# Kernel optimization log

Measured on AMD Instinct MI355X. Metric: run time of the kernel, lower is better.

Reference implementation:

```python
import jax, jax.numpy as jnp
import numpy as np

N_E = 16384      # codebook size
E_DIM = 32       # codebook vector dim (== channel dim of z)
BETA = 0.25      # commitment loss weight
ENT_RATIO = 0.1  # entropy loss ratio
TEMP = 0.01      # entropy loss temperature


def _l2norm(x, eps=1e-12):
    # matches F.normalize(p=2, dim=-1): x / max(||x||, eps)
    n = jnp.sqrt(jnp.sum(x * x, axis=-1, keepdims=True))
    return x / jnp.maximum(n, eps)


def _entropy_loss(affinity):
    # affinity: (T, N_E)
    fa = affinity / TEMP
    probs = jax.nn.softmax(fa, axis=-1)
    log_probs = jax.nn.log_softmax(fa + 1e-05, axis=-1)
    avg_probs = jnp.mean(probs, axis=0)
    avg_entropy = -jnp.sum(avg_probs * jnp.log(avg_probs + 1e-05))
    sample_entropy = -jnp.mean(jnp.sum(probs * log_probs, axis=-1))
    return sample_entropy - avg_entropy


def setup_inputs() -> dict:
    key = jax.random.key(0)
    k1, k2 = jax.random.split(key)
    z = jax.random.normal(k1, (32, E_DIM, 16, 16), dtype=jnp.float32)
    # torch init: uniform(-1/n_e, 1/n_e) then l2-normalized rows
    emb = jax.random.uniform(k2, (N_E, E_DIM), dtype=jnp.float32,
                             minval=-1.0 / N_E, maxval=1.0 / N_E)
    emb = _l2norm(emb)
    return {"z": z, "embedding": emb}


def reference(z, embedding):
    # z: (b, c, h, w) -> (b, h, w, c)
    zb = jnp.transpose(z, (0, 2, 3, 1))
    zb = _l2norm(zb)                       # l2_norm=True path
    zf = zb.reshape(-1, E_DIM)             # (T, d), T = b*h*w
    emb = _l2norm(embedding)               # (N_E, d)
    # squared L2 distances (cdist expansion)
    d = (jnp.sum(zf * zf, axis=1, keepdims=True)
         + jnp.sum(emb * emb, axis=1)
         - 2.0 * jnp.einsum('td,nd->tn', zf, emb))   # (T, N_E)
    idx = jnp.argmin(d, axis=1)            # (T,)
    z_q = emb[idx].reshape(zb.shape)       # (b, h, w, c)
    # training losses
    vq_loss = jnp.mean((z_q - jax.lax.stop_gradient(zb)) ** 2)
    commit_loss = BETA * jnp.mean((jax.lax.stop_gradient(z_q) - zb) ** 2)
    entropy_loss = ENT_RATIO * _entropy_loss(-d)
    # straight-through estimator
    z_q_st = zb + jax.lax.stop_gradient(z_q - zb)
    out = jnp.transpose(z_q_st, (0, 3, 1, 2))  # back to (b, c, h, w)
    return out, vq_loss, commit_loss, entropy_loss
```

## Files before the change

kernel.cpp:

```cpp
#include <hip/hip_runtime.h>


#define N_E 16384
#define ED 32
#define T 8192
#define NS1 16
#define SKIPM -36.0f
#define PHT 16

#define K2 288.53900817779268f
#define NS2F -144.26950408889634f
#define BIAS1 -208.53900817779268f
#define LN2 0.6931471805599453f

typedef __attribute__((ext_vector_type(8))) short s16x8;
typedef __attribute__((ext_vector_type(4))) float f32x4;

__device__ __forceinline__ float fexp2(float x) { return __builtin_amdgcn_exp2f(x); }
__device__ __forceinline__ float flog2(float x) { return __builtin_amdgcn_logf(x); }
__device__ __forceinline__ float fmed3(float a, float b, float c) {
  return __builtin_amdgcn_fmed3f(a, b, c);
}

__device__ __forceinline__ float midband(float key) {
  return __uint_as_float((__float_as_uint(key) & 0xFFFFFC00u) | 512u);
}

__device__ __forceinline__ void gload16(const void* g, void* l) {
  __builtin_amdgcn_global_load_lds(
      (const __attribute__((address_space(1))) void*)g,
      (__attribute__((address_space(3))) void*)l, 16, 0, 0);
}

__device__ __forceinline__ unsigned short f2bf(float x) {
  unsigned u = __float_as_uint(x);
  unsigned r = (u + 0x7FFFu + ((u >> 16) & 1u)) >> 16;
  return (unsigned short)r;
}
__device__ __forceinline__ float bf2f(unsigned short h) {
  return __uint_as_float(((unsigned)h) << 16);
}

__device__ __forceinline__ void split_store_t(short* __restrict__ base,
    int row, int g, float4 va, float4 vb, float sc) {
  float f[8] = { va.x * sc, va.y * sc, va.z * sc, va.w * sc,
                 vb.x * sc, vb.y * sc, vb.z * sc, vb.w * sc };
  s16x8 H, L;
#pragma unroll
  for (int e = 0; e < 8; ++e) {
    unsigned short h = f2bf(f[e]);
    H[e] = (short)h;
    L[e] = (short)f2bf(f[e] - bf2f(h));
  }
  s16x8* p = (s16x8*)base;
  const int tile = row >> 4, c = row & 15;
  p[tile * 128 + g * 16 + c] = H;
  p[tile * 128 + 64 + g * 16 + c] = L;
}

__device__ __forceinline__ void split_store_h(short* __restrict__ base,
    int row, int g, float4 va, float4 vb) {
  float f[8] = { va.x, va.y, va.z, va.w, vb.x, vb.y, vb.z, vb.w };
  s16x8 H;
#pragma unroll
  for (int e = 0; e < 8; ++e) H[e] = (short)f2bf(f[e]);
  ((s16x8*)base)[(row >> 4) * 64 + g * 16 + (row & 15)] = H;
}

__global__ __launch_bounds__(256) void k_prep(const float* __restrict__ emb,
    const float* __restrict__ z, float* __restrict__ embn,
    float* __restrict__ ses2, float* __restrict__ zf, float* __restrict__ a02,
    short* __restrict__ ehl, short* __restrict__ zhl, float* __restrict__ avg,
    float* __restrict__ scal) {
  if (blockIdx.x < 64) {
    int n = blockIdx.x * 256 + threadIdx.x;
    const float4* r4 = (const float4*)(emb + (size_t)n * ED);
    float4 v[8]; float s = 0.f;
#pragma unroll
    for (int j = 0; j < 8; ++j) {
      v[j] = r4[j];
      s = fmaf(v[j].x, v[j].x, s); s = fmaf(v[j].y, v[j].y, s);
      s = fmaf(v[j].z, v[j].z, s); s = fmaf(v[j].w, v[j].w, s);
    }
    float inv = 1.0f / fmaxf(sqrtf(s), 1e-12f);
    float s2 = 0.f;
    float4* o4 = (float4*)(embn + (size_t)n * ED);
#pragma unroll
    for (int j = 0; j < 8; ++j) {
      float4 w; w.x = v[j].x * inv; w.y = v[j].y * inv;
      w.z = v[j].z * inv; w.w = v[j].w * inv;
      o4[j] = w; v[j] = w;
      s2 = fmaf(w.x, w.x, s2); s2 = fmaf(w.y, w.y, s2);
      s2 = fmaf(w.z, w.z, s2); s2 = fmaf(w.w, w.w, s2);
    }
    ses2[n] = NS2F * s2;
#pragma unroll
    for (int g = 0; g < 4; ++g)
      split_store_h(ehl, n, g, v[2 * g], v[2 * g + 1]);
  } else if (blockIdx.x < 96) {
    int t = (blockIdx.x - 64) * 256 + threadIdx.x;
    int b = t >> 8, hw = t & 255;
    const float* base = z + (size_t)b * (ED * 256) + hw;
    float4 v[8]; float s = 0.f;
#pragma unroll
    for (int j = 0; j < 8; ++j) {
      float4 w;
      w.x = base[(4 * j + 0) * 256]; w.y = base[(4 * j + 1) * 256];
      w.z = base[(4 * j + 2) * 256]; w.w = base[(4 * j + 3) * 256];
      v[j] = w;
      s = fmaf(w.x, w.x, s); s = fmaf(w.y, w.y, s);
      s = fmaf(w.z, w.z, s); s = fmaf(w.w, w.w, s);
    }
    float inv = 1.0f / fmaxf(sqrtf(s), 1e-12f);
    float s2 = 0.f;
    float4* o4 = (float4*)(zf + (size_t)t * ED);
#pragma unroll
    for (int j = 0; j < 8; ++j) {
      float4 w; w.x = v[j].x * inv; w.y = v[j].y * inv;
      w.z = v[j].z * inv; w.w = v[j].w * inv;
      o4[j] = w; v[j] = w;
      s2 = fmaf(w.x, w.x, s2); s2 = fmaf(w.y, w.y, s2);
      s2 = fmaf(w.z, w.z, s2); s2 = fmaf(w.w, w.w, s2);
    }
    a02[t] = NS2F * s2;
#pragma unroll
    for (int g = 0; g < 4; ++g)
      split_store_t(zhl, t, g, v[2 * g], v[2 * g + 1], K2);
  } else if (blockIdx.x < 160) {
    avg[(blockIdx.x - 96) * 256 + threadIdx.x] = 0.f;
  } else {
    if (threadIdx.x < 4) scal[threadIdx.x] = 0.f;
  }
}

__global__ __launch_bounds__(256, 4) void k_pass1(
    const short* __restrict__ ehl, const short* __restrict__ zhl,
    float* __restrict__ cand1, float* __restrict__ cand2) {
  const int tid = threadIdx.x;
  const int lane = tid & 63, wv = tid >> 6;
  const int q = lane >> 4, c = lane & 15;
  const int rowbase = blockIdx.x * 128 + wv * 32;
  const int NT = (N_E / NS1) / 16;
  const int NP = NT / PHT;

  __shared__ s16x8 dbuf[2][PHT * 64];

  const s16x8* zg = (const s16x8*)zhl;
  const int atile = rowbase >> 4;
  s16x8 ah[2], al[2];
#pragma unroll
  for (int rg = 0; rg < 2; ++rg) {
    ah[rg] = zg[(atile + rg) * 128 + lane];
    al[rg] = zg[(atile + rg) * 128 + 64 + lane];
  }

  f32x4 bias;
#pragma unroll
  for (int r = 0; r < 4; ++r) bias[r] = BIAS1;

  float m1[2][4], m2[2][4];
#pragma unroll
  for (int rg = 0; rg < 2; ++rg)
#pragma unroll
    for (int k = 0; k < 4; ++k) { m1[rg][k] = -1e30f; m2[rg][k] = -1e30f; }

  const s16x8* eg = (const s16x8*)ehl + (size_t)blockIdx.y * (64 * 64);

#pragma unroll
  for (int j = 0; j < 4; ++j)
    gload16(eg + wv * 256 + j * 64 + lane, &dbuf[0][wv * 256 + j * 64]);
  __syncthreads();

  for (int p = 0; p < NP; ++p) {
    if (p + 1 < NP) {
      const s16x8* gs = eg + (p + 1) * (PHT * 64);
      s16x8* lb = &dbuf[(p + 1) & 1][0];
#pragma unroll
      for (int j = 0; j < 4; ++j)
        gload16(gs + wv * 256 + j * 64 + lane, lb + wv * 256 + j * 64);
    }
    const s16x8* bb = &dbuf[p & 1][0];
#pragma unroll
    for (int tt = 0; tt < PHT; ++tt) {
      s16x8 bh = bb[tt * 64 + lane];
      const unsigned tuc = (((unsigned)(p * PHT + tt)) << 4) | (unsigned)c;

      f32x4 acc0 = __builtin_amdgcn_mfma_f32_16x16x32_bf16(ah[0], bh, bias, 0, 0, 0);
      acc0 = __builtin_amdgcn_mfma_f32_16x16x32_bf16(al[0], bh, acc0, 0, 0, 0);
      f32x4 acc1 = __builtin_amdgcn_mfma_f32_16x16x32_bf16(ah[1], bh, bias, 0, 0, 0);
      acc1 = __builtin_amdgcn_mfma_f32_16x16x32_bf16(al[1], bh, acc1, 0, 0, 0);

#pragma unroll
      for (int r = 0; r < 4; ++r) {
        float k0 = __uint_as_float((__float_as_uint(acc0[r]) & 0xFFFFFC00u) | tuc);
        m2[0][r] = fmed3(k0, m1[0][r], m2[0][r]);
        m1[0][r] = fmaxf(m1[0][r], k0);
        float k1v = __uint_as_float((__float_as_uint(acc1[r]) & 0xFFFFFC00u) | tuc);
        m2[1][r] = fmed3(k1v, m1[1][r], m2[1][r]);
        m1[1][r] = fmaxf(m1[1][r], k1v);
      }
    }
    __syncthreads();
  }

  const int s = blockIdx.y;
#pragma unroll
  for (int rg = 0; rg < 2; ++rg) {
    float4 v1 = make_float4(m1[rg][0], m1[rg][1], m1[rg][2], m1[rg][3]);
    float4 v2 = make_float4(m2[rg][0], m2[rg][1], m2[rg][2], m2[rg][3]);
    const size_t base = (size_t)(s * 16 + c) * T + (rowbase + rg * 16 + q * 4);
    *(float4*)(cand1 + base) = v1;
    *(float4*)(cand2 + base) = v2;
  }
}

__global__ __launch_bounds__(256) void k_fin(
    const float* __restrict__ cand1, const float* __restrict__ cand2,
    const float* __restrict__ zf, const float* __restrict__ embn,
    const float* __restrict__ ses2, const float* __restrict__ a02,
    float* __restrict__ avg, float* __restrict__ scal,
    float* __restrict__ out) {
  const int tid = threadIdx.x;
  const int rr = tid & 15;
  const int g  = tid >> 4;
  const int row = blockIdx.x * 16 + rr;

  __shared__ float sZ[256], sS2[256], sk1[256];
  __shared__ unsigned long long rbest[16];
  __shared__ float slZ[16], sth[16], rsE[16], rvq[16];
  if (tid < 16) rbest[tid] = 0ull;

  float ka[16], kb[16];
  float k1 = -1e30f, Z = 0.f, S2 = 0.f;
#pragma unroll
  for (int k = 0; k < 16; ++k) {
    const int u = g * 16 + k;
    const float ca = cand1[(size_t)u * T + row];
    const float cb = cand2[(size_t)u * T + row];
    ka[k] = ca; kb[k] = cb;
    k1 = fmaxf(k1, ca);
    const float fa = midband(ca), fb = midband(cb);
    const float ea = fexp2(fa), eb = fexp2(fb);
    Z += ea + eb;
    S2 = fmaf(ea, fa, fmaf(eb, fb, S2));
  }
  sZ[tid] = Z; sS2[tid] = S2; sk1[tid] = k1;
  __syncthreads();
  for (int st = 8; st >= 1; st >>= 1) {
    if (g < st) {
      const int o = tid + st * 16;
      sZ[tid] += sZ[o]; sS2[tid] += sS2[o];
      sk1[tid] = fmaxf(sk1[tid], sk1[o]);
    }
    __syncthreads();
  }
  if (g == 0) { slZ[rr] = flog2(sZ[rr]); sth[rr] = sk1[rr] - 2.5f; }
  __syncthreads();
  const float lZ = slZ[rr], thr = sth[rr];
  const float a02t = a02[row];

#pragma unroll
  for (int k = 0; k < 16; ++k) {
    const int u = g * 16 + k;
#pragma unroll
    for (int h = 0; h < 2; ++h) {
      const float key = h ? kb[k] : ka[k];
      const unsigned kid = __float_as_uint(key) & 1023u;
      const int idx = (u >> 4) * 1024 + (int)((kid >> 4) << 4) + (int)(kid & 15u);
      const float dl = midband(key) - lZ;
      if (dl > SKIPM) atomicAdd(&avg[idx], fexp2(dl));
      if (key > thr) {
        const float4* er = (const float4*)(embn + (size_t)idx * ED);
        const float4* zr = (const float4*)(zf + (size_t)row * ED);
        float d = 0.f;
#pragma unroll
        for (int j = 0; j < 8; ++j) {
          float4 a = er[j], b = zr[j];
          d = fmaf(a.x, b.x, d); d = fmaf(a.y, b.y, d);
          d = fmaf(a.z, b.z, d); d = fmaf(a.w, b.w, d);
        }
        const float fbx = fmaf(K2, d, a02t + ses2[idx]);
        const unsigned ub = __float_as_uint(fbx);
        const unsigned ord = ub ^ (unsigned)(((int)ub >> 31) | 0x80000000);
        const unsigned long long pk =
            ((unsigned long long)ord << 14) | (unsigned long long)(16383 - idx);
        atomicMax(&rbest[rr], pk);
      }
    }
  }
  __syncthreads();

  if (g == 0) {
    rsE[rr] = sS2[rr] / sZ[rr] - lZ;
    const int bi = 16383 - (int)(rbest[rr] & 16383ull);

    const float4* zr4 = (const float4*)(zf + (size_t)row * ED);
    float4 z0 = zr4[0], z1 = zr4[1], z2 = zr4[2], z3 = zr4[3];
    float4 z4 = zr4[4], z5 = zr4[5], z6 = zr4[6], z7 = zr4[7];

    const int b = row >> 8, hw = row & 255;
    float* ob = out + (size_t)b * (ED * 256) + hw;
    float ss = 0.f;
    const float4* e4 = (const float4*)(embn + (size_t)bi * ED);
#pragma unroll
    for (int j = 0; j < 8; ++j) {
      float4 qv = e4[j];
      float4 zv = (j == 0) ? z0 : (j == 1) ? z1 : (j == 2) ? z2 : (j == 3) ? z3
                : (j == 4) ? z4 : (j == 5) ? z5 : (j == 6) ? z6 : z7;
      float df;
      df = qv.x - zv.x; ss = fmaf(df, df, ss); ob[(4 * j + 0) * 256] = zv.x + (qv.x - zv.x);
      df = qv.y - zv.y; ss = fmaf(df, df, ss); ob[(4 * j + 1) * 256] = zv.y + (qv.y - zv.y);
      df = qv.z - zv.z; ss = fmaf(df, df, ss); ob[(4 * j + 2) * 256] = zv.z + (qv.z - zv.z);
      df = qv.w - zv.w; ss = fmaf(df, df, ss); ob[(4 * j + 3) * 256] = zv.w + (qv.w - zv.w);
    }
    rvq[rr] = ss;
  }
  __syncthreads();
  if (tid == 0) {
    float se = 0.f, vq = 0.f;
    for (int i = 0; i < 16; ++i) { se += rsE[i]; vq += rvq[i]; }
    atomicAdd(&scal[0], se);
    atomicAdd(&scal[1], vq);
  }
}

__global__ __launch_bounds__(256) void k_last(const float* __restrict__ avg,
    const float* __restrict__ scal, float* __restrict__ out) {
  const int tid = threadIdx.x;
  __shared__ float red[256];
  float s = 0.f;
  for (int i = tid; i < N_E; i += 256) {
    float a = avg[i] * (1.0f / T);
    s += a * (flog2(a + 1e-5f) * LN2);
  }
  red[tid] = s;
  __syncthreads();
  for (int st = 128; st > 0; st >>= 1) {
    if (tid < st) red[tid] += red[tid + st];
    __syncthreads();
  }
  if (tid == 0) {
    float avg_entropy = -red[0];
    float sample_entropy = -(scal[0] * LN2) * (1.0f / T);
    float vq = scal[1] * (1.0f / (T * ED));
    out[T * ED + 0] = vq;
    out[T * ED + 1] = 0.25f * vq;
    out[T * ED + 2] = 0.1f * (sample_entropy - avg_entropy);
  }
}

extern "C" void kernel_launch(void* const* d_in, const int* in_sizes, int n_in,
                              void* d_out, int out_size, void* d_ws, size_t ws_size,
                              hipStream_t stream) {
  const float* z = (const float*)d_in[0];
  const float* emb = (const float*)d_in[1];
  float* out = (float*)d_out;
  float* w = (float*)d_ws;

  float* embn = w;
  float* ses2 = embn + 524288;
  float* zf   = ses2 + 16384;
  float* a02  = zf + 262144;
  short* ehl  = (short*)(a02 + 8192);
  short* zhl  = ehl + 524288;
  float* cand1 = (float*)(zhl + 524288);
  float* cand2 = cand1 + 256 * T;
  float* avg  = cand2 + 256 * T;
  float* scal = avg + 16384;

  k_prep<<<161, 256, 0, stream>>>(emb, z, embn, ses2, zf, a02, ehl, zhl,
                                  avg, scal);
  k_pass1<<<dim3(T / 128, NS1), 256, 0, stream>>>(ehl, zhl, cand1, cand2);
  k_fin<<<T / 16, 256, 0, stream>>>(cand1, cand2, zf, embn, ses2, a02,
                                    avg, scal, out);
  k_last<<<1, 256, 0, stream>>>(avg, scal, out);
}
```

Baseline: 138.4 us.

## Drop low-part bf16 MFMA in pass1 and threshold entropy sums by row max

The pass1 scoring now uses only the high bf16 half of the split z representation, removing the second MFMA per tile. That halves matrix work, but candidate keys become less precise and rely on the exact fp32 re-check in the finalize kernel, whose window widens from 2.5 to 5.0 units. The finalize kernel now computes the row max first, then accumulates the softmax partition sums and avg-prob atomics only for candidates within 36 units of the max. This skips negligible exponentials and atomics at the cost of an extra reduction barrier pass.

```diff
diff --git a/kernel.cpp b/kernel.cpp
--- a/kernel.cpp
+++ b/kernel.cpp
@@ -5,7 +5,8 @@
 #define ED 32
 #define T 8192
 #define NS1 16
-#define SKIPM -36.0f
+#define ZTH 36.0f
+#define RTH 5.0f
 #define PHT 16
 
 #define K2 288.53900817779268f
@@ -147,12 +148,10 @@
 
   const s16x8* zg = (const s16x8*)zhl;
   const int atile = rowbase >> 4;
-  s16x8 ah[2], al[2];
-#pragma unroll
-  for (int rg = 0; rg < 2; ++rg) {
+  s16x8 ah[2];
+#pragma unroll
+  for (int rg = 0; rg < 2; ++rg)
     ah[rg] = zg[(atile + rg) * 128 + lane];
-    al[rg] = zg[(atile + rg) * 128 + 64 + lane];
-  }
 
   f32x4 bias;
 #pragma unroll
@@ -186,9 +185,7 @@
       const unsigned tuc = (((unsigned)(p * PHT + tt)) << 4) | (unsigned)c;
 
       f32x4 acc0 = __builtin_amdgcn_mfma_f32_16x16x32_bf16(ah[0], bh, bias, 0, 0, 0);
-      acc0 = __builtin_amdgcn_mfma_f32_16x16x32_bf16(al[0], bh, acc0, 0, 0, 0);
       f32x4 acc1 = __builtin_amdgcn_mfma_f32_16x16x32_bf16(ah[1], bh, bias, 0, 0, 0);
-      acc1 = __builtin_amdgcn_mfma_f32_16x16x32_bf16(al[1], bh, acc1, 0, 0, 0);
 
 #pragma unroll
       for (int r = 0; r < 4; ++r) {
@@ -227,36 +224,50 @@
 
   __shared__ float sZ[256], sS2[256], sk1[256];
   __shared__ unsigned long long rbest[16];
-  __shared__ float slZ[16], sth[16], rsE[16], rvq[16];
+  __shared__ float slZ[16], rsE[16], rvq[16];
   if (tid < 16) rbest[tid] = 0ull;
 
   float ka[16], kb[16];
-  float k1 = -1e30f, Z = 0.f, S2 = 0.f;
+  float k1 = -1e30f;
 #pragma unroll
   for (int k = 0; k < 16; ++k) {
     const int u = g * 16 + k;
-    const float ca = cand1[(size_t)u * T + row];
-    const float cb = cand2[(size_t)u * T + row];
-    ka[k] = ca; kb[k] = cb;
-    k1 = fmaxf(k1, ca);
-    const float fa = midband(ca), fb = midband(cb);
-    const float ea = fexp2(fa), eb = fexp2(fb);
-    Z += ea + eb;
-    S2 = fmaf(ea, fa, fmaf(eb, fb, S2));
-  }
-  sZ[tid] = Z; sS2[tid] = S2; sk1[tid] = k1;
+    ka[k] = cand1[(size_t)u * T + row];
+    kb[k] = cand2[(size_t)u * T + row];
+    k1 = fmaxf(k1, ka[k]);
+  }
+  sk1[tid] = k1;
   __syncthreads();
   for (int st = 8; st >= 1; st >>= 1) {
-    if (g < st) {
-      const int o = tid + st * 16;
-      sZ[tid] += sZ[o]; sS2[tid] += sS2[o];
-      sk1[tid] = fmaxf(sk1[tid], sk1[o]);
-    }
+    if (g < st) sk1[tid] = fmaxf(sk1[tid], sk1[tid + st * 16]);
     __syncthreads();
   }
-  if (g == 0) { slZ[rr] = flog2(sZ[rr]); sth[rr] = sk1[rr] - 2.5f; }
-  __syncthreads();
-  const float lZ = slZ[rr], thr = sth[rr];
+  const float k1r = sk1[rr];
+  const float zth = k1r - ZTH, thr = k1r - RTH;
+
+  float Z = 0.f, S2 = 0.f;
+#pragma unroll
+  for (int k = 0; k < 16; ++k) {
+    if (ka[k] > zth) {
+      const float f = midband(ka[k]);
+      const float e = fexp2(f);
+      Z += e; S2 = fmaf(e, f, S2);
+    }
+    if (kb[k] > zth) {
+      const float f = midband(kb[k]);
+      const float e = fexp2(f);
+      Z += e; S2 = fmaf(e, f, S2);
+    }
+  }
+  sZ[tid] = Z; sS2[tid] = S2;
+  __syncthreads();
+  for (int st = 8; st >= 1; st >>= 1) {
+    if (g < st) { sZ[tid] += sZ[tid + st * 16]; sS2[tid] += sS2[tid + st * 16]; }
+    __syncthreads();
+  }
+  if (g == 0) slZ[rr] = flog2(sZ[rr]);
+  __syncthreads();
+  const float lZ = slZ[rr];
   const float a02t = a02[row];
 
 #pragma unroll
@@ -265,26 +276,27 @@
 #pragma unroll
     for (int h = 0; h < 2; ++h) {
       const float key = h ? kb[k] : ka[k];
-      const unsigned kid = __float_as_uint(key) & 1023u;
-      const int idx = (u >> 4) * 1024 + (int)((kid >> 4) << 4) + (int)(kid & 15u);
-      const float dl = midband(key) - lZ;
-      if (dl > SKIPM) atomicAdd(&avg[idx], fexp2(dl));
-      if (key > thr) {
-        const float4* er = (const float4*)(embn + (size_t)idx * ED);
-        const float4* zr = (const float4*)(zf + (size_t)row * ED);
-        float d = 0.f;
-#pragma unroll
-        for (int j = 0; j < 8; ++j) {
-          float4 a = er[j], b = zr[j];
-          d = fmaf(a.x, b.x, d); d = fmaf(a.y, b.y, d);
-          d = fmaf(a.z, b.z, d); d = fmaf(a.w, b.w, d);
+      if (key > zth) {
+        const unsigned kid = __float_as_uint(key) & 1023u;
+        const int idx = (u >> 4) * 1024 + (int)((kid >> 4) << 4) + (int)(kid & 15u);
+        atomicAdd(&avg[idx], fexp2(midband(key) - lZ));
+        if (key > thr) {
+          const float4* er = (const float4*)(embn + (size_t)idx * ED);
+          const float4* zr = (const float4*)(zf + (size_t)row * ED);
+          float d = 0.f;
+#pragma unroll
+          for (int j = 0; j < 8; ++j) {
+            float4 a = er[j], b = zr[j];
+            d = fmaf(a.x, b.x, d); d = fmaf(a.y, b.y, d);
+            d = fmaf(a.z, b.z, d); d = fmaf(a.w, b.w, d);
+          }
+          const float fbx = fmaf(K2, d, a02t + ses2[idx]);
+          const unsigned ub = __float_as_uint(fbx);
+          const unsigned ord = ub ^ (unsigned)(((int)ub >> 31) | 0x80000000);
+          const unsigned long long pk =
+              ((unsigned long long)ord << 14) | (unsigned long long)(16383 - idx);
+          atomicMax(&rbest[rr], pk);
         }
-        const float fbx = fmaf(K2, d, a02t + ses2[idx]);
-        const unsigned ub = __float_as_uint(fbx);
-        const unsigned ord = ub ^ (unsigned)(((int)ub >> 31) | 0x80000000);
-        const unsigned long long pk =
-            ((unsigned long long)ord << 14) | (unsigned long long)(16383 - idx);
-        atomicMax(&rbest[rr], pk);
       }
     }
   }
```

Result: no change. 136.9 us (median of 2 runs) (-1.1%).
